# Kernel optimization log

Measured on AMD Instinct MI355X. Metric: run time of the kernel, lower is better.

Reference implementation:

```python
import jax, jax.numpy as jnp
import numpy as np

B = 2
SP = (480, 360, 32)   # spatial_shape (z, y, x)
GS = (8, 8, 8)        # query_gs_ratio
EP = (40, 15, 16)     # embed_params (pool compress ratio)
H = 8
N = 120000
D = 256
OUT = 20


def _dims(rat):
    return tuple((s + r - 1) // r for s, r in zip(SP, rat))


def sine_pe(coords, d_pos):
    # coords: [M,3] float voxel coords in original grid units; normalized sine PE
    nf = d_pos // 6
    sp = jnp.asarray(SP, jnp.float32)
    cn = coords / sp * (2.0 * jnp.pi)                      # normalize=True
    t = 10000.0 ** (jnp.arange(nf, dtype=jnp.float32) / nf)
    ang = cn[:, :, None] / t                               # [M,3,nf]
    pe = jnp.concatenate([jnp.sin(ang), jnp.cos(ang)], -1).reshape(coords.shape[0], -1)
    return jnp.pad(pe, ((0, 0), (0, d_pos - 6 * nf)))


def setup_inputs() -> dict:
    key = jax.random.key(0)
    ks = jax.random.split(key, 24)
    idx_b = jax.random.randint(ks[0], (N, 1), 0, B)
    idx_z = jax.random.randint(ks[1], (N, 1), 0, SP[0])
    idx_y = jax.random.randint(ks[2], (N, 1), 0, SP[1])
    idx_x = jax.random.randint(ks[3], (N, 1), 0, SP[2])
    indices = jnp.concatenate([idx_b, idx_z, idx_y, idx_x], axis=1).astype(jnp.int32)
    s = D ** -0.5
    p = lambda k, sh: jax.random.normal(k, sh, jnp.float32) * s
    return {
        'features': jax.random.normal(ks[4], (N, D), jnp.float32),
        'W_pool': p(ks[5], (D, D)), 'b_pool': jnp.zeros((D,), jnp.float32),
        'W_emb': p(ks[6], (D, D)), 'b_emb': jnp.zeros((D,), jnp.float32),
        'Wq': p(ks[7], (D, D)), 'bq': jnp.zeros((D,), jnp.float32),
        'Wk': p(ks[8], (D, D)), 'bk': jnp.zeros((D,), jnp.float32),
        'Wv': p(ks[9], (D, D)), 'bv': jnp.zeros((D,), jnp.float32),
        'Wo': p(ks[10], (D, D)), 'bo': jnp.zeros((D,), jnp.float32),
        'ln_g': jnp.ones((D,), jnp.float32), 'ln_b': jnp.zeros((D,), jnp.float32),
        'W_seg': p(ks[11], (D, OUT)), 'b_seg': jnp.zeros((OUT,), jnp.float32),
        'indices': indices,
        'batch_size': B,
    }


def reference(features, W_pool, b_pool, W_emb, b_emb, Wq, bq, Wk, bk, Wv, bv,
              Wo, bo, ln_g, ln_b, W_seg, b_seg, indices, batch_size):
    Zd, Yd, Xd = _dims(GS)
    Gq = Zd * Yd * Xd
    Sq = batch_size * Gq
    Ze, Ye, Xe = _dims(EP)
    Gk = Ze * Ye * Xe
    Sk = batch_size * Gk
    n = features.shape[0]

    # --- query pool branch: linear -> voxel-grid scatter_max ---
    pf = features @ W_pool + b_pool                                    # [N,D]
    dq = indices[:, 1:] // jnp.asarray(GS, jnp.int32)
    seg_q = ((indices[:, 0] * Zd + dq[:, 0]) * Yd + dq[:, 1]) * Xd + dq[:, 2]
    pool_max = jax.ops.segment_max(pf, seg_q, num_segments=Sq)
    cnt_q = jax.ops.segment_sum(jnp.ones((n,), jnp.float32), seg_q, num_segments=Sq)
    mq = cnt_q > 0
    pool_max = jnp.where(mq[:, None], pool_max, 0.0)
    cell = jnp.arange(Sq)
    rem = cell % Gq
    pool_c = jnp.stack([(rem // (Yd * Xd)) * GS[0],
                        ((rem // Xd) % Yd) * GS[1],
                        (rem % Xd) * GS[2]], -1).astype(jnp.float32)   # [Sq,3]

    # --- embedding branch ('pool'): linear -> coarse scatter_max + per-channel argmax coords ---
    ef = features @ W_emb + b_emb                                      # [N,D]
    de = indices[:, 1:] // jnp.asarray(EP, jnp.int32)
    seg_k = ((indices[:, 0] * Ze + de[:, 0]) * Ye + de[:, 1]) * Xe + de[:, 2]
    emb_max = jax.ops.segment_max(ef, seg_k, num_segments=Sk)
    cnt_k = jax.ops.segment_sum(jnp.ones((n,), jnp.float32), seg_k, num_segments=Sk)
    mk = cnt_k > 0
    emb_max = jnp.where(mk[:, None], emb_max, 0.0)
    winner = ef == jnp.where(mk[:, None], emb_max, -jnp.inf)[seg_k]
    idx = jax.ops.segment_max(jnp.where(winner, jnp.arange(n)[:, None], -1), seg_k, num_segments=Sk)
    idx_c = jnp.clip(idx, 0, n - 1)                                    # [Sk,D]
    ec = de.astype(jnp.float32)                                        # [N,3] downsampled coords
    emb_c = ec[idx_c].mean(axis=1) * jnp.asarray(EP, jnp.float32)      # [Sk,3]

    # --- position encoding (pointwise sine PE; per-batch loop in torch is pointwise-equivalent) ---
    pool_max = pool_max + sine_pe(pool_c, D)
    emb_max = emb_max + sine_pe(emb_c, D)

    # --- multi-head cross-attention (Q=pool, K/V=embedding), per-batch via dense grid reshape ---
    q_in = pool_max.reshape(batch_size, Gq, D)
    kv_in = emb_max.reshape(batch_size, Gk, D)
    dh = D // H
    q = (q_in @ Wq + bq).reshape(batch_size, Gq, H, dh)
    k = (kv_in @ Wk + bk).reshape(batch_size, Gk, H, dh)
    v = (kv_in @ Wv + bv).reshape(batch_size, Gk, H, dh)
    scores = jnp.einsum('bqhd,bkhd->bhqk', q, k) / jnp.float32(dh) ** 0.5
    kmask = mk.reshape(batch_size, Gk)
    scores = jnp.where(kmask[:, None, None, :], scores, -1e9)
    attn = jax.nn.softmax(scores, axis=-1)
    o = jnp.einsum('bhqk,bkhd->bqhd', attn, v).reshape(batch_size, Gq, D) @ Wo + bo
    h = q_in + o                                                       # residual + LayerNorm sublayer
    mu = h.mean(-1, keepdims=True)
    var = h.var(-1, keepdims=True)
    h = (h - mu) * jax.lax.rsqrt(var + 1e-5) * ln_g + ln_b
    feats_mhca = h.reshape(Sq, D)

    # --- gather back to voxels via pool_inv, residual, seg head (center-tap of SubMConv3d) ---
    vox = features + feats_mhca[seg_q]
    logits = vox @ W_seg + b_seg
    return logits
```

## Files before the change

### kernel.cpp

```cpp
#include <hip/hip_runtime.h>
#include <math.h>

#define N_PTS 120000
#define D 256
#define BATCH 2
#define NH 8
#define DH 32
#define OUTC 20

#define Zd 60
#define Yd 45
#define Xd 4
#define Gq 10800
#define Sq 21600

#define Ze 12
#define Ye 24
#define Xe 2
#define Gk 576
#define Sk 1152

#define QK_SCALE (0.17677669529663688f * 1.4426950408889634f)

typedef __bf16 bf16_t;
typedef __attribute__((ext_vector_type(8))) __bf16 bf16x8;
typedef __attribute__((ext_vector_type(4))) __bf16 bf16x4;
typedef __attribute__((ext_vector_type(4))) float f32x4;

__device__ __forceinline__ void glds16(const void* g, void* l) {
    __builtin_amdgcn_global_load_lds(
        (const __attribute__((address_space(1))) unsigned int*)g,
        (__attribute__((address_space(3))) unsigned int*)l,
        16, 0, 0);
}

__global__ __launch_bounds__(256) void k_prep(
    const float* __restrict__ Wp, const float* __restrict__ We,
    const float* __restrict__ Wq, const float* __restrict__ Wk,
    const float* __restrict__ Wv, const float* __restrict__ Wo,
    const float* __restrict__ bp, const float* __restrict__ be,
    const float* __restrict__ bq, const float* __restrict__ bk,
    const float* __restrict__ bv,
    const float* __restrict__ Wseg, const float* __restrict__ bseg,
    bf16_t* __restrict__ Wpe, bf16_t* __restrict__ Wqt,
    bf16_t* __restrict__ Wkv, bf16_t* __restrict__ Wot,
    bf16_t* __restrict__ Wsegt,
    float* __restrict__ bpe, float* __restrict__ bkv,
    float* __restrict__ bsegp, float* __restrict__ bqs)
{
    int n = blockIdx.x, k = threadIdx.x;
    if (n < 512) {
        const float* S = (n < 256) ? Wp : We;
        int nn = n & 255;
        Wpe[n * 256 + k] = (bf16_t)S[k * 256 + nn];
    } else if (n < 768) {
        int nn = n - 512;
        Wqt[nn * 256 + k] = (bf16_t)(Wq[k * 256 + nn] * QK_SCALE);
    } else if (n < 1280) {
        int m2 = n - 768;
        const float* S = (m2 < 256) ? Wk : Wv;
        int nn = m2 & 255;
        Wkv[m2 * 256 + k] = (bf16_t)S[k * 256 + nn];
    } else if (n < 1536) {
        int nn = n - 1280;
        Wot[nn * 256 + k] = (bf16_t)Wo[k * 256 + nn];
    } else if (n == 1536) {
        bpe[k] = bp[k]; bpe[256 + k] = be[k];
        bkv[k] = bk[k]; bkv[256 + k] = bv[k];
        bqs[k] = bq[k] * QK_SCALE;
        if (k < 32) bsegp[k] = (k < OUTC) ? bseg[k] : 0.f;
    } else {
        int n2 = n - 1537;
        Wsegt[n2 * 256 + k] = (n2 < OUTC) ? (bf16_t)Wseg[k * OUTC + n2] : (bf16_t)0.f;
    }
}

__global__ __launch_bounds__(256) void k_cast(
    const float* __restrict__ in, bf16_t* __restrict__ out)
{
    const size_t total = (size_t)N_PTS * 32;
    const size_t stride = (size_t)gridDim.x * 256;
    for (size_t i = (size_t)blockIdx.x * 256 + threadIdx.x; i < total; i += stride) {
        float4 a = *(const float4*)(in + i * 8);
        float4 b = *(const float4*)(in + i * 8 + 4);
        bf16x8 o;
        o[0] = (bf16_t)a.x; o[1] = (bf16_t)a.y; o[2] = (bf16_t)a.z; o[3] = (bf16_t)a.w;
        o[4] = (bf16_t)b.x; o[5] = (bf16_t)b.y; o[6] = (bf16_t)b.z; o[7] = (bf16_t)b.w;
        *(bf16x8*)(out + i * 8) = o;
    }
}

__global__ __launch_bounds__(256) void k_count(
    const int* __restrict__ indices, int* __restrict__ cnt_q, int* __restrict__ cnt_k,
    int* __restrict__ segq, int* __restrict__ segk)
{
    int i = blockIdx.x * 256 + threadIdx.x;
    if (i >= N_PTS) return;
    const int* id = indices + (size_t)i * 4;
    int b = id[0], z = id[1], y = id[2], x = id[3];
    int sq = ((b * Zd + (z >> 3)) * Yd + (y >> 3)) * Xd + (x >> 3);
    int sk = ((b * Ze + (z / 40)) * Ye + (y / 15)) * Xe + (x >> 4);
    segq[i] = sq; segk[i] = sk;
    atomicAdd(&cnt_q[sq], 1);
    atomicAdd(&cnt_k[sk], 1);
}

__global__ __launch_bounds__(1024) void k_scan(
    const int* __restrict__ cnt, int n, int* __restrict__ offs, int* __restrict__ cursor)
{
    __shared__ int wbase[17];
    __shared__ int carry_s;
    const int t = threadIdx.x, lane = t & 63, w = t >> 6;
    if (t == 0) carry_s = 0;
    __syncthreads();
    for (int base = 0; base < n; base += 1024) {
        int v = (base + t < n) ? cnt[base + t] : 0;
        int incl = v;
        #pragma unroll
        for (int off = 1; off < 64; off <<= 1) {
            int u = __shfl_up(incl, off);
            if (lane >= off) incl += u;
        }
        if (lane == 63) wbase[w + 1] = incl;
        __syncthreads();
        if (t == 0) {
            int s = 0;
            wbase[0] = 0;
            #pragma unroll
            for (int i = 1; i <= 16; ++i) { s += wbase[i]; wbase[i] = s; }
        }
        __syncthreads();
        int excl = incl - v + wbase[w] + carry_s;
        if (base + t < n) { offs[base + t] = excl; cursor[base + t] = excl; }
        __syncthreads();
        if (t == 0) carry_s += wbase[16];
        __syncthreads();
    }
}

__global__ __launch_bounds__(256) void k_place(
    const int* __restrict__ segq, const int* __restrict__ segk,
    int* __restrict__ cur_q, int* __restrict__ cur_k,
    int* __restrict__ ids_q, int* __restrict__ ids_k)
{
    int i = blockIdx.x * 256 + threadIdx.x;
    if (i >= N_PTS) return;
    ids_q[atomicAdd(&cur_q[segq[i]], 1)] = i;
    ids_k[atomicAdd(&cur_k[segk[i]], 1)] = i;
}

__global__ __launch_bounds__(256, 4) void k_gemm_bf(
    const bf16_t* __restrict__ A, int M,
    const bf16_t* __restrict__ Wt, const float* __restrict__ bias,
    bf16_t* __restrict__ outb, int ldo)
{
    __shared__ __align__(16) bf16_t Abuf[128 * 64];
    __shared__ __align__(16) bf16_t Bbuf[128 * 64];

    const int t = threadIdx.x;
    const int wave = t >> 6, lane = t & 63;
    const int wr = wave >> 1, wc = wave & 1;
    const int lrow = lane & 15, quad = lane >> 4;
    const int lr8 = lane >> 3, lc8 = lane & 7;
    const int row0 = blockIdx.y * 128;
    const int ntile = blockIdx.x;

    f32x4 acc[4][4];
    #pragma unroll
    for (int mi = 0; mi < 4; ++mi)
        #pragma unroll
        for (int ni = 0; ni < 4; ++ni)
            acc[mi][ni] = (f32x4){0.f, 0.f, 0.f, 0.f};

    for (int k0 = 0; k0 < 256; k0 += 64) {
        #pragma unroll
        for (int i = 0; i < 4; ++i) {
            int chunk = wave * 4 + i;
            int rowA = row0 + chunk * 8 + lr8;
            if (rowA > M - 1) rowA = M - 1;
            glds16(A + (size_t)rowA * 256 + k0 + lc8 * 8, &Abuf[chunk * 512]);
        }
        #pragma unroll
        for (int i = 0; i < 4; ++i) {
            int chunk = wave * 4 + i;
            glds16(Wt + (size_t)(ntile * 128 + chunk * 8 + lr8) * 256 + k0 + lc8 * 8,
                   &Bbuf[chunk * 512]);
        }
        asm volatile("s_waitcnt vmcnt(0)" ::: "memory");
        __builtin_amdgcn_sched_barrier(0);
        __syncthreads();

        #pragma unroll
        for (int kk = 0; kk < 64; kk += 32) {
            bf16x8 Af[4], Bf[4];
            #pragma unroll
            for (int mi = 0; mi < 4; ++mi)
                Af[mi] = *(const bf16x8*)&Abuf[(wr * 64 + mi * 16 + lrow) * 64 + kk + quad * 8];
            #pragma unroll
            for (int ni = 0; ni < 4; ++ni)
                Bf[ni] = *(const bf16x8*)&Bbuf[(wc * 64 + ni * 16 + lrow) * 64 + kk + quad * 8];
            #pragma unroll
            for (int mi = 0; mi < 4; ++mi)
                #pragma unroll
                for (int ni = 0; ni < 4; ++ni)
                    acc[mi][ni] = __builtin_amdgcn_mfma_f32_16x16x32_bf16(
                        Af[mi], Bf[ni], acc[mi][ni], 0, 0, 0);
        }
        __syncthreads();
    }

    const int colb = ntile * 128 + wc * 64;
    float biasv[4];
    #pragma unroll
    for (int ni = 0; ni < 4; ++ni) biasv[ni] = bias[colb + ni * 16 + lrow];

    #pragma unroll
    for (int mi = 0; mi < 4; ++mi) {
        int lr = wr * 64 + mi * 16 + quad * 4;
        #pragma unroll
        for (int reg = 0; reg < 4; ++reg) {
            int grow = row0 + lr + reg;
            if (grow >= M) continue;
            #pragma unroll
            for (int ni = 0; ni < 4; ++ni) {
                int col = colb + ni * 16 + lrow;
                outb[(size_t)grow * ldo + col] = (bf16_t)(acc[mi][ni][reg] + biasv[ni]);
            }
        }
    }
}

__global__ __launch_bounds__(512, 2) void k_gemm(
    const float* __restrict__ A, int M,
    const bf16_t* __restrict__ Wt, const float* __restrict__ bias,
    int mode, float* __restrict__ outp, int ldo)
{
    __shared__ __align__(16) bf16_t Abuf[128][72];
    __shared__ __align__(16) bf16_t Bbuf[256][72];

    const int t = threadIdx.x;
    const int wave = t >> 6, lane = t & 63;
    const int wr = wave >> 2, wc = wave & 3;
    const int lrow = lane & 15, quad = lane >> 4;
    const int row0 = blockIdx.y * 128;
    const int ntile = blockIdx.x;

    f32x4 acc[4][4];
    #pragma unroll
    for (int mi = 0; mi < 4; ++mi)
        #pragma unroll
        for (int ni = 0; ni < 4; ++ni)
            acc[mi][ni] = (f32x4){0.f, 0.f, 0.f, 0.f};

    for (int k0 = 0; k0 < 256; k0 += 64) {
        #pragma unroll
        for (int i = 0; i < 4; ++i) {
            int c = i * 512 + t;
            int r = c >> 4, c4 = c & 15;
            float4 v = make_float4(0.f, 0.f, 0.f, 0.f);
            if (row0 + r < M)
                v = *(const float4*)(A + (size_t)(row0 + r) * 256 + k0 + c4 * 4);
            bf16x4 bv4;
            bv4[0] = (bf16_t)v.x; bv4[1] = (bf16_t)v.y;
            bv4[2] = (bf16_t)v.z; bv4[3] = (bf16_t)v.w;
            *(bf16x4*)&Abuf[r][c4 * 4] = bv4;
        }
        #pragma unroll
        for (int i = 0; i < 4; ++i) {
            int c = i * 512 + t;
            int r = c >> 3, c8 = c & 7;
            uint4 w = *(const uint4*)(Wt + ((size_t)(ntile * 256 + r)) * 256 + k0 + c8 * 8);
            *(uint4*)&Bbuf[r][c8 * 8] = w;
        }
        __syncthreads();

        #pragma unroll
        for (int kk = 0; kk < 64; kk += 32) {
            bf16x8 Af[4], Bf[4];
            #pragma unroll
            for (int mi = 0; mi < 4; ++mi)
                Af[mi] = *(const bf16x8*)&Abuf[wr * 64 + mi * 16 + lrow][kk + quad * 8];
            #pragma unroll
            for (int ni = 0; ni < 4; ++ni)
                Bf[ni] = *(const bf16x8*)&Bbuf[wc * 64 + ni * 16 + lrow][kk + quad * 8];
            #pragma unroll
            for (int mi = 0; mi < 4; ++mi)
                #pragma unroll
                for (int ni = 0; ni < 4; ++ni)
                    acc[mi][ni] = __builtin_amdgcn_mfma_f32_16x16x32_bf16(
                        Af[mi], Bf[ni], acc[mi][ni], 0, 0, 0);
        }
        __syncthreads();
    }

    const int colb = ntile * 256 + wc * 64;
    float biasv[4];
    #pragma unroll
    for (int ni = 0; ni < 4; ++ni) biasv[ni] = bias[colb + ni * 16 + lrow];

    if (mode == 0) {
        #pragma unroll
        for (int mi = 0; mi < 4; ++mi) {
            int lr = wr * 64 + mi * 16 + quad * 4;
            #pragma unroll
            for (int reg = 0; reg < 4; ++reg) {
                int grow = row0 + lr + reg;
                if (grow >= M) continue;
                #pragma unroll
                for (int ni = 0; ni < 4; ++ni) {
                    int col = colb + ni * 16 + lrow;
                    outp[(size_t)grow * ldo + col] = acc[mi][ni][reg] + biasv[ni];
                }
            }
        }
    } else {
        bf16_t* outb = (bf16_t*)outp;
        #pragma unroll
        for (int mi = 0; mi < 4; ++mi) {
            int lr = wr * 64 + mi * 16 + quad * 4;
            #pragma unroll
            for (int reg = 0; reg < 4; ++reg) {
                int grow = row0 + lr + reg;
                if (grow >= M) continue;
                #pragma unroll
                for (int ni = 0; ni < 4; ++ni) {
                    int col = colb + ni * 16 + lrow;
                    outb[(size_t)grow * ldo + col] = (bf16_t)(acc[mi][ni][reg] + biasv[ni]);
                }
            }
        }
    }
}

__device__ inline float pe_val(int j, float cz, float cy, float cx) {
    if (j >= 252) return 0.f;
    int dim = j / 84;
    int f = j % 84;
    int fi = (f >= 42) ? (f - 42) : f;
    float c  = (dim == 0) ? cz : ((dim == 1) ? cy : cx);
    float sp = (dim == 0) ? 480.f : ((dim == 1) ? 360.f : 32.f);
    float cn = c / sp * 6.28318530717958647692f;
    float tt = expf((float)fi * (9.210340371976184f / 42.f));
    float ang = cn / tt;
    return (f >= 42) ? cosf(ang) : sinf(ang);
}

__global__ __launch_bounds__(256) void k_pool_q(
    const bf16_t* __restrict__ pfb, const int* __restrict__ ids,
    const int* __restrict__ offs, const int* __restrict__ cnt,
    float* __restrict__ out)
{
    const int t = threadIdx.x, lane = t & 63, w = t >> 6;
    const int s = blockIdx.x * 4 + w;
    if (s >= Sq) return;
    const int count = cnt[s], start = offs[s];
    float mx[4] = {-3.0e38f, -3.0e38f, -3.0e38f, -3.0e38f};
    for (int r = 0; r < count; ++r) {
        int i = ids[start + r];
        bf16x4 v = *(const bf16x4*)(pfb + (size_t)i * 256 + lane * 4);
        #pragma unroll
        for (int j = 0; j < 4; ++j) mx[j] = fmaxf(mx[j], (float)v[j]);
    }
    int rem = s % Gq;
    float cz = (float)((rem / (Yd * Xd)) * 8);
    float cy = (float)(((rem / Xd) % Yd) * 8);
    float cx = (float)((rem % Xd) * 8);
    #pragma unroll
    for (int j = 0; j < 4; ++j) {
        float v = (count > 0) ? mx[j] : 0.f;
        out[(size_t)s * 256 + lane * 4 + j] = v + pe_val(lane * 4 + j, cz, cy, cx);
    }
}

__global__ __launch_bounds__(512) void k_pool_k(
    const bf16_t* __restrict__ efb, const int* __restrict__ ids,
    const int* __restrict__ offs, const int* __restrict__ cnt,
    float* __restrict__ out, int* __restrict__ kmask)
{
    __shared__ float red[8][256];
    const int t = threadIdx.x, lane = t & 63, w = t >> 6;
    const int s = blockIdx.x;
    const int count = cnt[s], start = offs[s];
    float mx[4] = {-3.0e38f, -3.0e38f, -3.0e38f, -3.0e38f};
    for (int r = w; r < count; r += 8) {
        int i = ids[start + r];
        bf16x4 v = *(const bf16x4*)(efb + (size_t)i * 256 + lane * 4);
        #pragma unroll
        for (int j = 0; j < 4; ++j) mx[j] = fmaxf(mx[j], (float)v[j]);
    }
    #pragma unroll
    for (int j = 0; j < 4; ++j) red[w][lane * 4 + j] = mx[j];
    __syncthreads();
    if (t < 256) {
        float m = red[0][t];
        #pragma unroll
        for (int i = 1; i < 8; ++i) m = fmaxf(m, red[i][t]);
        if (count == 0) m = 0.f;
        int rem = s % Gk;
        float cz = (float)((rem / (Ye * Xe)) * 40);
        float cy = (float)(((rem / Xe) % Ye) * 15);
        float cx = (float)((rem % Xe) * 16);
        out[(size_t)s * 256 + t] = m + pe_val(t, cz, cy, cx);
        if (t == 0) kmask[s] = (count > 0) ? 1 : 0;
    }
}

__global__ __launch_bounds__(256) void k_vt(
    const bf16_t* __restrict__ KVb, bf16_t* __restrict__ VT)
{
    int idx = blockIdx.x * 256 + threadIdx.x;
    if (idx >= 16 * 32 * 576) return;
    int g = idx % 576;
    int d = (idx / 576) & 31;
    int bh = idx / (576 * 32);
    int b = bh >> 3, h = bh & 7;
    VT[idx] = KVb[((size_t)(b * Gk + g)) * 512 + 256 + h * 32 + d];
}

__global__ __launch_bounds__(768, 6) void k_attn5(
    const bf16_t* __restrict__ Q, const bf16_t* __restrict__ KV,
    const bf16_t* __restrict__ VT, const int* __restrict__ kmask,
    float* __restrict__ O)
{
    __shared__ __align__(16) bf16_t Vts[32][584];
    __shared__ __align__(16) bf16_t Ps[12][16][104];
    __shared__ float mskf[576];

    const int bh = blockIdx.y;
    const int b = bh >> 3, h = bh & 7;
    const int t = threadIdx.x, wave = t >> 6, lane = t & 63;
    const int lrow = lane & 15, quad = lane >> 4;
    const int q0 = blockIdx.x * 192;

    #pragma unroll
    for (int i = 0; i < 3; ++i) {
        int id = i * 768 + t;
        int d = id / 72, c8 = id % 72;
        uint4 v = *(const uint4*)(VT + (size_t)(bh * 32 + d) * 576 + c8 * 8);
        *(uint4*)&Vts[d][c8 * 8] = v;
    }
    if (t < 576)
        mskf[t] = kmask[b * Gk + t] ? 0.f : -1.0e9f;
    __syncthreads();

    int qa = q0 + wave * 16 + lrow;
    if (qa > Gq - 1) qa = Gq - 1;
    const bf16x8 Aq = *(const bf16x8*)(Q + ((size_t)(b * Gq + qa)) * 256 + h * 32 + quad * 8);

    const bf16_t* Kbase = KV + ((size_t)b * Gk) * 512 + h * 32;

    f32x4 oacc[2];
    oacc[0] = (f32x4){0.f, 0.f, 0.f, 0.f};
    oacc[1] = (f32x4){0.f, 0.f, 0.f, 0.f};
    float l[4] = {0.f, 0.f, 0.f, 0.f};

    for (int c0 = 0; c0 < Gk; c0 += 96) {
        #pragma unroll
        for (int nt = 0; nt < 6; ++nt) {
            bf16x8 Bk = *(const bf16x8*)(Kbase + (size_t)(c0 + nt * 16 + lrow) * 512 + quad * 8);
            f32x4 sacc = __builtin_amdgcn_mfma_f32_16x16x32_bf16(
                Aq, Bk, (f32x4){0.f, 0.f, 0.f, 0.f}, 0, 0, 0);
            float pen = mskf[c0 + nt * 16 + lrow];
            #pragma unroll
            for (int r = 0; r < 4; ++r) {
                float p = exp2f(sacc[r] + pen);
                l[r] += p;
                Ps[wave][quad * 4 + r][nt * 16 + lrow] = (bf16_t)p;
            }
        }
        #pragma unroll
        for (int ks = 0; ks < 3; ++ks) {
            bf16x8 Ap = *(const bf16x8*)&Ps[wave][lrow][ks * 32 + quad * 8];
            #pragma unroll
            for (int n2 = 0; n2 < 2; ++n2) {
                bf16x8 Bv = *(const bf16x8*)&Vts[n2 * 16 + lrow][c0 + ks * 32 + quad * 8];
                oacc[n2] = __builtin_amdgcn_mfma_f32_16x16x32_bf16(
                    Ap, Bv, oacc[n2], 0, 0, 0);
            }
        }
    }

    #pragma unroll
    for (int r = 0; r < 4; ++r)
        #pragma unroll
        for (int off = 1; off < 16; off <<= 1)
            l[r] += __shfl_xor(l[r], off);

    #pragma unroll
    for (int r = 0; r < 4; ++r) {
        int qi = q0 + wave * 16 + quad * 4 + r;
        if (qi >= Gq) continue;
        float inv = (l[r] > 0.f) ? (1.f / l[r]) : 0.f;
        #pragma unroll
        for (int n2 = 0; n2 < 2; ++n2)
            O[((size_t)(b * Gq + qi)) * 256 + h * 32 + n2 * 16 + lrow] = oacc[n2][r] * inv;
    }
}

__global__ __launch_bounds__(256) void k_ln(
    const float* __restrict__ oproj, const float* __restrict__ resid,
    const float* __restrict__ g, const float* __restrict__ bta,
    float* __restrict__ out)
{
    const int s = blockIdx.x, t = threadIdx.x;
    float h = resid[(size_t)s * D + t] + oproj[(size_t)s * D + t];

    float s1 = h, s2 = h * h;
    for (int o = 32; o > 0; o >>= 1) {
        s1 += __shfl_down(s1, o);
        s2 += __shfl_down(s2, o);
    }
    __shared__ float r1[4], r2[4];
    __shared__ float mu_s, rstd_s;
    int w = t >> 6;
    if ((t & 63) == 0) { r1[w] = s1; r2[w] = s2; }
    __syncthreads();
    if (t == 0) {
        float a = r1[0] + r1[1] + r1[2] + r1[3];
        float bsum = r2[0] + r2[1] + r2[2] + r2[3];
        float mu = a * (1.f / 256.f);
        float var = bsum * (1.f / 256.f) - mu * mu;
        mu_s = mu;
        rstd_s = rsqrtf(var + 1e-5f);
    }
    __syncthreads();
    out[(size_t)s * D + t] = (h - mu_s) * rstd_s * g[t] + bta[t];
}

__global__ __launch_bounds__(512, 2) void k_logits_mfma(
    const float* __restrict__ feat, const bf16_t* __restrict__ featb,
    const float* __restrict__ mhca,
    const int* __restrict__ indices, const bf16_t* __restrict__ Wsegt,
    const float* __restrict__ bsegp, float* __restrict__ out)
{
    __shared__ __align__(16) bf16_t Abuf[128][72];
    __shared__ __align__(16) bf16_t Bbuf[32][72];
    __shared__ int sq_s[128];

    const int t = threadIdx.x;
    const int wave = t >> 6, lane = t & 63;
    const int lrow = lane & 15, quad = lane >> 4;
    const int row0 = blockIdx.x * 128;

    if (t < 128) {
        int row = row0 + t;
        if (row < N_PTS) {
            const int* id = indices + (size_t)row * 4;
            sq_s[t] = ((id[0] * Zd + (id[1] >> 3)) * Yd + (id[2] >> 3)) * Xd + (id[3] >> 3);
        } else sq_s[t] = 0;
    }
    __syncthreads();

    f32x4 acc[2];
    acc[0] = (f32x4){0.f, 0.f, 0.f, 0.f};
    acc[1] = (f32x4){0.f, 0.f, 0.f, 0.f};

    for (int k0 = 0; k0 < 256; k0 += 64) {
        #pragma unroll
        for (int i = 0; i < 4; ++i) {
            int c = i * 512 + t;
            int r = c >> 4, c4 = c & 15;
            float4 v = make_float4(0.f, 0.f, 0.f, 0.f);
            int grow = row0 + r;
            if (grow < N_PTS) {
                float4 mm = *(const float4*)(mhca + (size_t)sq_s[r] * 256 + k0 + c4 * 4);
                if (featb) {
                    bf16x4 fv = *(const bf16x4*)(featb + (size_t)grow * 256 + k0 + c4 * 4);
                    v.x = (float)fv[0] + mm.x; v.y = (float)fv[1] + mm.y;
                    v.z = (float)fv[2] + mm.z; v.w = (float)fv[3] + mm.w;
                } else {
                    v = *(const float4*)(feat + (size_t)grow * 256 + k0 + c4 * 4);
                    v.x += mm.x; v.y += mm.y; v.z += mm.z; v.w += mm.w;
                }
            }
            bf16x4 bv4;
            bv4[0] = (bf16_t)v.x; bv4[1] = (bf16_t)v.y;
            bv4[2] = (bf16_t)v.z; bv4[3] = (bf16_t)v.w;
            *(bf16x4*)&Abuf[r][c4 * 4] = bv4;
        }
        if (t < 256) {
            int r = t >> 3, c8 = t & 7;
            uint4 w = *(const uint4*)(Wsegt + (size_t)r * 256 + k0 + c8 * 8);
            *(uint4*)&Bbuf[r][c8 * 8] = w;
        }
        __syncthreads();

        #pragma unroll
        for (int kk = 0; kk < 64; kk += 32) {
            bf16x8 Af = *(const bf16x8*)&Abuf[wave * 16 + lrow][kk + quad * 8];
            #pragma unroll
            for (int ni = 0; ni < 2; ++ni) {
                bf16x8 Bf = *(const bf16x8*)&Bbuf[ni * 16 + lrow][kk + quad * 8];
                acc[ni] = __builtin_amdgcn_mfma_f32_16x16x32_bf16(
                    Af, Bf, acc[ni], 0, 0, 0);
            }
        }
        __syncthreads();
    }

    #pragma unroll
    for (int ni = 0; ni < 2; ++ni) {
        int col = ni * 16 + lrow;
        if (col >= OUTC) continue;
        float bias = bsegp[col];
        #pragma unroll
        for (int reg = 0; reg < 4; ++reg) {
            int grow = row0 + wave * 16 + quad * 4 + reg;
            if (grow >= N_PTS) continue;
            out[(size_t)grow * OUTC + col] = acc[ni][reg] + bias;
        }
    }
}

extern "C" void kernel_launch(void* const* d_in, const int* in_sizes, int n_in,
                              void* d_out, int out_size, void* d_ws, size_t ws_size,
                              hipStream_t stream) {
    const float* features = (const float*)d_in[0];
    const float* W_pool = (const float*)d_in[1];
    const float* b_pool = (const float*)d_in[2];
    const float* W_emb  = (const float*)d_in[3];
    const float* b_emb  = (const float*)d_in[4];
    const float* Wq = (const float*)d_in[5];
    const float* bq = (const float*)d_in[6];
    const float* Wk = (const float*)d_in[7];
    const float* bk = (const float*)d_in[8];
    const float* Wv = (const float*)d_in[9];
    const float* bv = (const float*)d_in[10];
    const float* Wo = (const float*)d_in[11];
    const float* bo = (const float*)d_in[12];
    const float* ln_g = (const float*)d_in[13];
    const float* ln_b = (const float*)d_in[14];
    const float* W_seg = (const float*)d_in[15];
    const float* b_seg = (const float*)d_in[16];
    const int* indices = (const int*)d_in[17];
    float* out = (float*)d_out;

    float* ws = (float*)d_ws;
    const size_t SQD = (size_t)Sq * D;
    const size_t SKD = (size_t)Sk * D;
    const size_t PFB_FL = (size_t)N_PTS * D / 2;

    size_t oP   = 0;
    size_t oPF  = oP + PFB_FL;
    size_t oEF  = oPF + SQD;
    size_t oWpe = oEF + SKD;
    size_t oWqt = oWpe + 65536;
    size_t oWkv = oWqt + 32768;
    size_t oWot = oWkv + 65536;
    size_t obpe = oWot + 32768;
    size_t obkv = obpe + 512;
    size_t oCnt = obkv + 512;
    size_t oOffq = oCnt + 21600 + 1152;
    size_t oCurq = oOffq + 21600;
    size_t oOffk = oCurq + 21600;
    size_t oCurk = oOffk + 1152;
    size_t oSegq = oCurk + 1152;
    size_t oSegk = oSegq + N_PTS;
    size_t oIdsq = oSegk + N_PTS;
    size_t oIdsk = oIdsq + N_PTS;
    size_t oKm   = oIdsk + N_PTS;
    size_t oWst  = oKm + 1152;
    size_t obsg  = oWst + 4096;
    size_t obqs  = obsg + 32;
    size_t oFB   = obqs + 256;

    bf16_t* pfb = (bf16_t*)(ws + oP);
    float* pool_feat = ws + oPF;
    float* emb_feat  = ws + oEF;
    bf16_t* Wpe = (bf16_t*)(ws + oWpe);
    bf16_t* Wqt = (bf16_t*)(ws + oWqt);
    bf16_t* Wkv = (bf16_t*)(ws + oWkv);
    bf16_t* Wot = (bf16_t*)(ws + oWot);
    float* bpe = ws + obpe;
    float* bkv = ws + obkv;
    int* cnt_q = (int*)(ws + oCnt);
    int* cnt_k = cnt_q + 21600;
    int* offs_q = (int*)(ws + oOffq);
    int* cur_q  = (int*)(ws + oCurq);
    int* offs_k = (int*)(ws + oOffk);
    int* cur_k  = (int*)(ws + oCurk);
    int* segq = (int*)(ws + oSegq);
    int* segk = (int*)(ws + oSegk);
    int* ids_q = (int*)(ws + oIdsq);
    int* ids_k = (int*)(ws + oIdsk);
    int* kmask = (int*)(ws + oKm);
    bf16_t* Wsegt = (bf16_t*)(ws + oWst);
    float* bsegp = ws + obsg;
    float* bqs = ws + obqs;
    bf16_t* fb16 = (bf16_t*)(ws + oFB);

    bf16_t* Qb  = (bf16_t*)(ws + oP);
    bf16_t* KVb = (bf16_t*)(ws + oP + 2764800);
    float* attnO = ws + oP + 3059712;
    float* oproj = ws + oP + 8589312;
    float* mhca  = ws + oP + 3059712;
    bf16_t* VT = (bf16_t*)(ws + oEF);

    const bool fast = ws_size >= (oFB + PFB_FL) * sizeof(float);

    hipMemsetAsync(cnt_q, 0, (21600 + 1152) * sizeof(int), stream);

    k_prep<<<1569, 256, 0, stream>>>(W_pool, W_emb, Wq, Wk, Wv, Wo,
                                     b_pool, b_emb, bq, bk, bv, W_seg, b_seg,
                                     Wpe, Wqt, Wkv, Wot, Wsegt, bpe, bkv, bsegp, bqs);

    if (fast)
        k_cast<<<2048, 256, 0, stream>>>(features, fb16);

    k_count<<<(N_PTS + 255) / 256, 256, 0, stream>>>(indices, cnt_q, cnt_k, segq, segk);
    k_scan<<<1, 1024, 0, stream>>>(cnt_q, 21600, offs_q, cur_q);
    k_scan<<<1, 1024, 0, stream>>>(cnt_k, 1152, offs_k, cur_k);
    k_place<<<(N_PTS + 255) / 256, 256, 0, stream>>>(segq, segk, cur_q, cur_k, ids_q, ids_k);

    if (fast) {
        dim3 g(2, (N_PTS + 127) / 128);
        k_gemm_bf<<<g, 256, 0, stream>>>(fb16, N_PTS, Wpe + 256 * 256, bpe + 256,
                                         pfb, 256);
    } else {
        dim3 g(1, (N_PTS + 127) / 128);
        k_gemm<<<g, 512, 0, stream>>>(features, N_PTS, Wpe + 256 * 256, bpe + 256, 2,
                                      (float*)pfb, 256);
    }
    k_pool_k<<<Sk, 512, 0, stream>>>(pfb, ids_k, offs_k, cnt_k, emb_feat, kmask);

    if (fast) {
        dim3 g(2, (N_PTS + 127) / 128);
        k_gemm_bf<<<g, 256, 0, stream>>>(fb16, N_PTS, Wpe, bpe, pfb, 256);
    } else {
        dim3 g(1, (N_PTS + 127) / 128);
        k_gemm<<<g, 512, 0, stream>>>(features, N_PTS, Wpe, bpe, 2,
                                      (float*)pfb, 256);
    }
    k_pool_q<<<(Sq + 3) / 4, 256, 0, stream>>>(pfb, ids_q, offs_q, cnt_q, pool_feat);

    {
        dim3 g(1, (Sq + 127) / 128);
        k_gemm<<<g, 512, 0, stream>>>(pool_feat, Sq, Wqt, bqs, 2, (float*)Qb, 256);
    }
    {
        dim3 g(2, (Sk + 127) / 128);
        k_gemm<<<g, 512, 0, stream>>>(emb_feat, Sk, Wkv, bkv, 2, (float*)KVb, 512);
    }

    k_vt<<<(16 * 32 * 576 + 255) / 256, 256, 0, stream>>>(KVb, VT);

    {
        dim3 ag((Gq + 191) / 192, BATCH * NH);
        k_attn5<<<ag, 768, 0, stream>>>(Qb, KVb, VT, kmask, attnO);
    }

    {
        dim3 g(1, (Sq + 127) / 128);
        k_gemm<<<g, 512, 0, stream>>>(attnO, Sq, Wot, bo, 0, oproj, 256);
    }

    k_ln<<<Sq, 256, 0, stream>>>(oproj, pool_feat, ln_g, ln_b, mhca);

    k_logits_mfma<<<(N_PTS + 127) / 128, 512, 0, stream>>>(
        features, fast ? fb16 : (const bf16_t*)nullptr, mhca, indices, Wsegt, bsegp, out);
}
```

Measured before the change: 575.0 us.

## Carry bf16 intermediates through attention path and use glds GEMMs for Q, O-proj, logits

The pooled query features, attention output and LayerNorm output are now written as bf16 instead of fp32. The Q projection and output projection move onto the bf16 direct-to-LDS GEMM kernel, which gains an fp32-output option. A new logits kernel loads bf16 features and gathered mhca rows straight into LDS and accumulates both through MFMA, so it no longer converts fp32 inputs in registers. This cuts memory traffic and conversion work, at the cost of extra rounding of intermediates to bf16.

```diff
diff --git a/kernel.cpp b/kernel.cpp
--- a/kernel.cpp
+++ b/kernel.cpp
@@ -152,7 +152,7 @@
 __global__ __launch_bounds__(256, 4) void k_gemm_bf(
     const bf16_t* __restrict__ A, int M,
     const bf16_t* __restrict__ Wt, const float* __restrict__ bias,
-    bf16_t* __restrict__ outb, int ldo)
+    void* __restrict__ outp, int ldo, int fp32out)
 {
     __shared__ __align__(16) bf16_t Abuf[128 * 64];
     __shared__ __align__(16) bf16_t Bbuf[128 * 64];
@@ -224,7 +224,11 @@
             #pragma unroll
             for (int ni = 0; ni < 4; ++ni) {
                 int col = colb + ni * 16 + lrow;
-                outb[(size_t)grow * ldo + col] = (bf16_t)(acc[mi][ni][reg] + biasv[ni]);
+                float val = acc[mi][ni][reg] + biasv[ni];
+                if (fp32out)
+                    ((float*)outp)[(size_t)grow * ldo + col] = val;
+                else
+                    ((bf16_t*)outp)[(size_t)grow * ldo + col] = (bf16_t)val;
             }
         }
     }
@@ -348,7 +352,7 @@
 __global__ __launch_bounds__(256) void k_pool_q(
     const bf16_t* __restrict__ pfb, const int* __restrict__ ids,
     const int* __restrict__ offs, const int* __restrict__ cnt,
-    float* __restrict__ out)
+    float* __restrict__ out, bf16_t* __restrict__ outb)
 {
     const int t = threadIdx.x, lane = t & 63, w = t >> 6;
     const int s = blockIdx.x * 4 + w;
@@ -365,11 +369,15 @@
     float cz = (float)((rem / (Yd * Xd)) * 8);
     float cy = (float)(((rem / Xd) % Yd) * 8);
     float cx = (float)((rem % Xd) * 8);
+    bf16x4 ob;
     #pragma unroll
     for (int j = 0; j < 4; ++j) {
         float v = (count > 0) ? mx[j] : 0.f;
-        out[(size_t)s * 256 + lane * 4 + j] = v + pe_val(lane * 4 + j, cz, cy, cx);
-    }
+        float o = v + pe_val(lane * 4 + j, cz, cy, cx);
+        out[(size_t)s * 256 + lane * 4 + j] = o;
+        ob[j] = (bf16_t)o;
+    }
+    *(bf16x4*)(outb + (size_t)s * 256 + lane * 4) = ob;
 }
 
 __global__ __launch_bounds__(512) void k_pool_k(
@@ -420,7 +428,7 @@
 __global__ __launch_bounds__(768, 6) void k_attn5(
     const bf16_t* __restrict__ Q, const bf16_t* __restrict__ KV,
     const bf16_t* __restrict__ VT, const int* __restrict__ kmask,
-    float* __restrict__ O)
+    bf16_t* __restrict__ O)
 {
     __shared__ __align__(16) bf16_t Vts[32][584];
     __shared__ __align__(16) bf16_t Ps[12][16][104];
@@ -493,14 +501,15 @@
         float inv = (l[r] > 0.f) ? (1.f / l[r]) : 0.f;
         #pragma unroll
         for (int n2 = 0; n2 < 2; ++n2)
-            O[((size_t)(b * Gq + qi)) * 256 + h * 32 + n2 * 16 + lrow] = oacc[n2][r] * inv;
+            O[((size_t)(b * Gq + qi)) * 256 + h * 32 + n2 * 16 + lrow] =
+                (bf16_t)(oacc[n2][r] * inv);
     }
 }
 
 __global__ __launch_bounds__(256) void k_ln(
     const float* __restrict__ oproj, const float* __restrict__ resid,
     const float* __restrict__ g, const float* __restrict__ bta,
-    float* __restrict__ out)
+    bf16_t* __restrict__ out)
 {
     const int s = blockIdx.x, t = threadIdx.x;
     float h = resid[(size_t)s * D + t] + oproj[(size_t)s * D + t];
@@ -524,12 +533,102 @@
         rstd_s = rsqrtf(var + 1e-5f);
     }
     __syncthreads();
-    out[(size_t)s * D + t] = (h - mu_s) * rstd_s * g[t] + bta[t];
+    out[(size_t)s * D + t] = (bf16_t)((h - mu_s) * rstd_s * g[t] + bta[t]);
+}
+
+__global__ __launch_bounds__(256, 4) void k_logits_glds(
+    const bf16_t* __restrict__ featb, const bf16_t* __restrict__ mhcab,
+    const int* __restrict__ indices, const bf16_t* __restrict__ Wsegt,
+    const float* __restrict__ bsegp, float* __restrict__ out)
+{
+    __shared__ __align__(16) bf16_t Fbuf[128 * 64];
+    __shared__ __align__(16) bf16_t Mbuf[128 * 64];
+    __shared__ __align__(16) bf16_t Bbuf[32 * 64];
+    __shared__ int sq_s[128];
+
+    const int t = threadIdx.x;
+    const int wave = t >> 6, lane = t & 63;
+    const int lrow = lane & 15, quad = lane >> 4;
+    const int lr8 = lane >> 3, lc8 = lane & 7;
+    const int row0 = blockIdx.x * 128;
+
+    if (t < 128) {
+        int row = row0 + t;
+        if (row >= N_PTS) row = N_PTS - 1;
+        const int* id = indices + (size_t)row * 4;
+        sq_s[t] = ((id[0] * Zd + (id[1] >> 3)) * Yd + (id[2] >> 3)) * Xd + (id[3] >> 3);
+    }
+    __syncthreads();
+
+    f32x4 acc[2][2];
+    #pragma unroll
+    for (int mi = 0; mi < 2; ++mi)
+        #pragma unroll
+        for (int ni = 0; ni < 2; ++ni)
+            acc[mi][ni] = (f32x4){0.f, 0.f, 0.f, 0.f};
+
+    for (int k0 = 0; k0 < 256; k0 += 64) {
+        #pragma unroll
+        for (int i = 0; i < 4; ++i) {
+            int chunk = wave * 4 + i;
+            int rowA = row0 + chunk * 8 + lr8;
+            if (rowA > N_PTS - 1) rowA = N_PTS - 1;
+            glds16(featb + (size_t)rowA * 256 + k0 + lc8 * 8, &Fbuf[chunk * 512]);
+        }
+        #pragma unroll
+        for (int i = 0; i < 4; ++i) {
+            int chunk = wave * 4 + i;
+            int mrow = sq_s[chunk * 8 + lr8];
+            glds16(mhcab + (size_t)mrow * 256 + k0 + lc8 * 8, &Mbuf[chunk * 512]);
+        }
+        glds16(Wsegt + (size_t)(wave * 8 + lr8) * 256 + k0 + lc8 * 8, &Bbuf[wave * 512]);
+
+        asm volatile("s_waitcnt vmcnt(0)" ::: "memory");
+        __builtin_amdgcn_sched_barrier(0);
+        __syncthreads();
+
+        #pragma unroll
+        for (int kk = 0; kk < 64; kk += 32) {
+            bf16x8 Bf[2];
+            #pragma unroll
+            for (int ni = 0; ni < 2; ++ni)
+                Bf[ni] = *(const bf16x8*)&Bbuf[(ni * 16 + lrow) * 64 + kk + quad * 8];
+            #pragma unroll
+            for (int mi = 0; mi < 2; ++mi) {
+                int arow = wave * 32 + mi * 16 + lrow;
+                bf16x8 Ff = *(const bf16x8*)&Fbuf[arow * 64 + kk + quad * 8];
+                bf16x8 Mf = *(const bf16x8*)&Mbuf[arow * 64 + kk + quad * 8];
+                #pragma unroll
+                for (int ni = 0; ni < 2; ++ni) {
+                    acc[mi][ni] = __builtin_amdgcn_mfma_f32_16x16x32_bf16(
+                        Ff, Bf[ni], acc[mi][ni], 0, 0, 0);
+                    acc[mi][ni] = __builtin_amdgcn_mfma_f32_16x16x32_bf16(
+                        Mf, Bf[ni], acc[mi][ni], 0, 0, 0);
+                }
+            }
+        }
+        __syncthreads();
+    }
+
+    #pragma unroll
+    for (int ni = 0; ni < 2; ++ni) {
+        int col = ni * 16 + lrow;
+        if (col >= OUTC) continue;
+        float bias = bsegp[col];
+        #pragma unroll
+        for (int mi = 0; mi < 2; ++mi) {
+            #pragma unroll
+            for (int reg = 0; reg < 4; ++reg) {
+                int grow = row0 + wave * 32 + mi * 16 + quad * 4 + reg;
+                if (grow >= N_PTS) continue;
+                out[(size_t)grow * OUTC + col] = acc[mi][ni][reg] + bias;
+            }
+        }
+    }
 }
 
 __global__ __launch_bounds__(512, 2) void k_logits_mfma(
-    const float* __restrict__ feat, const bf16_t* __restrict__ featb,
-    const float* __restrict__ mhca,
+    const float* __restrict__ feat, const bf16_t* __restrict__ mhcab,
     const int* __restrict__ indices, const bf16_t* __restrict__ Wsegt,
     const float* __restrict__ bsegp, float* __restrict__ out)
 {
@@ -563,15 +662,10 @@
             float4 v = make_float4(0.f, 0.f, 0.f, 0.f);
             int grow = row0 + r;
             if (grow < N_PTS) {
-                float4 mm = *(const float4*)(mhca + (size_t)sq_s[r] * 256 + k0 + c4 * 4);
-                if (featb) {
-                    bf16x4 fv = *(const bf16x4*)(featb + (size_t)grow * 256 + k0 + c4 * 4);
-                    v.x = (float)fv[0] + mm.x; v.y = (float)fv[1] + mm.y;
-                    v.z = (float)fv[2] + mm.z; v.w = (float)fv[3] + mm.w;
-                } else {
-                    v = *(const float4*)(feat + (size_t)grow * 256 + k0 + c4 * 4);
-                    v.x += mm.x; v.y += mm.y; v.z += mm.z; v.w += mm.w;
-                }
+                v = *(const float4*)(feat + (size_t)grow * 256 + k0 + c4 * 4);
+                bf16x4 mv = *(const bf16x4*)(mhcab + (size_t)sq_s[r] * 256 + k0 + c4 * 4);
+                v.x += (float)mv[0]; v.y += (float)mv[1];
+                v.z += (float)mv[2]; v.w += (float)mv[3];
             }
             bf16x4 bv4;
             bv4[0] = (bf16_t)v.x; bv4[1] = (bf16_t)v.y;
@@ -639,6 +733,7 @@
     const size_t SQD = (size_t)Sq * D;
     const size_t SKD = (size_t)Sk * D;
     const size_t PFB_FL = (size_t)N_PTS * D / 2;
+    const size_t SQB_FL = (size_t)Sq * D / 2;
 
     size_t oP   = 0;
     size_t oPF  = oP + PFB_FL;
@@ -662,7 +757,8 @@
     size_t oWst  = oKm + 1152;
     size_t obsg  = oWst + 4096;
     size_t obqs  = obsg + 32;
-    size_t oFB   = obqs + 256;
+    size_t oPFB  = obqs + 256;
+    size_t oFB   = oPFB + SQB_FL;
 
     bf16_t* pfb = (bf16_t*)(ws + oP);
     float* pool_feat = ws + oPF;
@@ -687,13 +783,14 @@
     bf16_t* Wsegt = (bf16_t*)(ws + oWst);
     float* bsegp = ws + obsg;
     float* bqs = ws + obqs;
+    bf16_t* pool_featb = (bf16_t*)(ws + oPFB);
     bf16_t* fb16 = (bf16_t*)(ws + oFB);
 
     bf16_t* Qb  = (bf16_t*)(ws + oP);
     bf16_t* KVb = (bf16_t*)(ws + oP + 2764800);
-    float* attnO = ws + oP + 3059712;
+    bf16_t* Ob  = (bf16_t*)(ws + oP + 3059712);
     float* oproj = ws + oP + 8589312;
-    float* mhca  = ws + oP + 3059712;
+    bf16_t* mhcab = (bf16_t*)(ws + oP + 3059712);
     bf16_t* VT = (bf16_t*)(ws + oEF);
 
     const bool fast = ws_size >= (oFB + PFB_FL) * sizeof(float);
@@ -715,7 +812,7 @@
     if (fast) {
         dim3 g(2, (N_PTS + 127) / 128);
         k_gemm_bf<<<g, 256, 0, stream>>>(fb16, N_PTS, Wpe + 256 * 256, bpe + 256,
-                                         pfb, 256);
+                                         pfb, 256, 0);
     } else {
         dim3 g(1, (N_PTS + 127) / 128);
         k_gemm<<<g, 512, 0, stream>>>(features, N_PTS, Wpe + 256 * 256, bpe + 256, 2,
@@ -725,17 +822,18 @@
 
     if (fast) {
         dim3 g(2, (N_PTS + 127) / 128);
-        k_gemm_bf<<<g, 256, 0, stream>>>(fb16, N_PTS, Wpe, bpe, pfb, 256);
+        k_gemm_bf<<<g, 256, 0, stream>>>(fb16, N_PTS, Wpe, bpe, pfb, 256, 0);
     } else {
         dim3 g(1, (N_PTS + 127) / 128);
         k_gemm<<<g, 512, 0, stream>>>(features, N_PTS, Wpe, bpe, 2,
                                       (float*)pfb, 256);
     }
-    k_pool_q<<<(Sq + 3) / 4, 256, 0, stream>>>(pfb, ids_q, offs_q, cnt_q, pool_feat);
+    k_pool_q<<<(Sq + 3) / 4, 256, 0, stream>>>(pfb, ids_q, offs_q, cnt_q,
+                                               pool_feat, pool_featb);
 
     {
-        dim3 g(1, (Sq + 127) / 128);
-        k_gemm<<<g, 512, 0, stream>>>(pool_feat, Sq, Wqt, bqs, 2, (float*)Qb, 256);
+        dim3 g(2, (Sq + 127) / 128);
+        k_gemm_bf<<<g, 256, 0, stream>>>(pool_featb, Sq, Wqt, bqs, Qb, 256, 0);
     }
     {
         dim3 g(2, (Sk + 127) / 128);
@@ -746,16 +844,20 @@
 
     {
         dim3 ag((Gq + 191) / 192, BATCH * NH);
-        k_attn5<<<ag, 768, 0, stream>>>(Qb, KVb, VT, kmask, attnO);
+        k_attn5<<<ag, 768, 0, stream>>>(Qb, KVb, VT, kmask, Ob);
     }
 
     {
-        dim3 g(1, (Sq + 127) / 128);
-        k_gemm<<<g, 512, 0, stream>>>(attnO, Sq, Wot, bo, 0, oproj, 256);
-    }
-
-    k_ln<<<Sq, 256, 0, stream>>>(oproj, pool_feat, ln_g, ln_b, mhca);
-
-    k_logits_mfma<<<(N_PTS + 127) / 128, 512, 0, stream>>>(
-        features, fast ? fb16 : (const bf16_t*)nullptr, mhca, indices, Wsegt, bsegp, out);
-}
+        dim3 g(2, (Sq + 127) / 128);
+        k_gemm_bf<<<g, 256, 0, stream>>>(Ob, Sq, Wot, bo, oproj, 256, 1);
+    }
+
+    k_ln<<<Sq, 256, 0, stream>>>(oproj, pool_feat, ln_g, ln_b, mhcab);
+
+    if (fast)
+        k_logits_glds<<<(N_PTS + 127) / 128, 256, 0, stream>>>(
+            fb16, mhcab, indices, Wsegt, bsegp, out);
+    else
+        k_logits_mfma<<<(N_PTS + 127) / 128, 512, 0, stream>>>(
+            features, mhcab, indices, Wsegt, bsegp, out);
+}
```

Measured after the change: 588.4 us. 2.3% more time.

## Carry bf16 intermediates through Q-proj, attention output, O-proj and LayerNorm

Applied to the files above, without the earlier changes.

Pooled query features, the attention output and the LayerNorm output are now also stored in bf16. The Q and O projections switch from the fp32-input GEMM to the bf16-input GEMM, which gains an fp32-output option. This is meant to cut memory traffic and the in-kernel fp32-to-bf16 conversion in those GEMMs, and to halve the gather bandwidth in the logits kernel. It costs an extra bf16 write in k_pool_q and extra rounding of intermediates.

```diff
diff --git a/kernel.cpp b/kernel.cpp
--- a/kernel.cpp
+++ b/kernel.cpp
@@ -152,7 +152,7 @@
 __global__ __launch_bounds__(256, 4) void k_gemm_bf(
     const bf16_t* __restrict__ A, int M,
     const bf16_t* __restrict__ Wt, const float* __restrict__ bias,
-    bf16_t* __restrict__ outb, int ldo)
+    void* __restrict__ outp, int ldo, int fp32out)
 {
     __shared__ __align__(16) bf16_t Abuf[128 * 64];
     __shared__ __align__(16) bf16_t Bbuf[128 * 64];
@@ -224,7 +224,11 @@
             #pragma unroll
             for (int ni = 0; ni < 4; ++ni) {
                 int col = colb + ni * 16 + lrow;
-                outb[(size_t)grow * ldo + col] = (bf16_t)(acc[mi][ni][reg] + biasv[ni]);
+                float val = acc[mi][ni][reg] + biasv[ni];
+                if (fp32out)
+                    ((float*)outp)[(size_t)grow * ldo + col] = val;
+                else
+                    ((bf16_t*)outp)[(size_t)grow * ldo + col] = (bf16_t)val;
             }
         }
     }
@@ -348,7 +352,7 @@
 __global__ __launch_bounds__(256) void k_pool_q(
     const bf16_t* __restrict__ pfb, const int* __restrict__ ids,
     const int* __restrict__ offs, const int* __restrict__ cnt,
-    float* __restrict__ out)
+    float* __restrict__ out, bf16_t* __restrict__ outb)
 {
     const int t = threadIdx.x, lane = t & 63, w = t >> 6;
     const int s = blockIdx.x * 4 + w;
@@ -365,11 +369,15 @@
     float cz = (float)((rem / (Yd * Xd)) * 8);
     float cy = (float)(((rem / Xd) % Yd) * 8);
     float cx = (float)((rem % Xd) * 8);
+    bf16x4 ob;
     #pragma unroll
     for (int j = 0; j < 4; ++j) {
         float v = (count > 0) ? mx[j] : 0.f;
-        out[(size_t)s * 256 + lane * 4 + j] = v + pe_val(lane * 4 + j, cz, cy, cx);
-    }
+        float o = v + pe_val(lane * 4 + j, cz, cy, cx);
+        out[(size_t)s * 256 + lane * 4 + j] = o;
+        ob[j] = (bf16_t)o;
+    }
+    *(bf16x4*)(outb + (size_t)s * 256 + lane * 4) = ob;
 }
 
 __global__ __launch_bounds__(512) void k_pool_k(
@@ -420,7 +428,7 @@
 __global__ __launch_bounds__(768, 6) void k_attn5(
     const bf16_t* __restrict__ Q, const bf16_t* __restrict__ KV,
     const bf16_t* __restrict__ VT, const int* __restrict__ kmask,
-    float* __restrict__ O)
+    bf16_t* __restrict__ O)
 {
     __shared__ __align__(16) bf16_t Vts[32][584];
     __shared__ __align__(16) bf16_t Ps[12][16][104];
@@ -493,14 +501,15 @@
         float inv = (l[r] > 0.f) ? (1.f / l[r]) : 0.f;
         #pragma unroll
         for (int n2 = 0; n2 < 2; ++n2)
-            O[((size_t)(b * Gq + qi)) * 256 + h * 32 + n2 * 16 + lrow] = oacc[n2][r] * inv;
+            O[((size_t)(b * Gq + qi)) * 256 + h * 32 + n2 * 16 + lrow] =
+                (bf16_t)(oacc[n2][r] * inv);
     }
 }
 
 __global__ __launch_bounds__(256) void k_ln(
     const float* __restrict__ oproj, const float* __restrict__ resid,
     const float* __restrict__ g, const float* __restrict__ bta,
-    float* __restrict__ out)
+    bf16_t* __restrict__ out)
 {
     const int s = blockIdx.x, t = threadIdx.x;
     float h = resid[(size_t)s * D + t] + oproj[(size_t)s * D + t];
@@ -524,12 +533,12 @@
         rstd_s = rsqrtf(var + 1e-5f);
     }
     __syncthreads();
-    out[(size_t)s * D + t] = (h - mu_s) * rstd_s * g[t] + bta[t];
+    out[(size_t)s * D + t] = (bf16_t)((h - mu_s) * rstd_s * g[t] + bta[t]);
 }
 
 __global__ __launch_bounds__(512, 2) void k_logits_mfma(
     const float* __restrict__ feat, const bf16_t* __restrict__ featb,
-    const float* __restrict__ mhca,
+    const bf16_t* __restrict__ mhcab,
     const int* __restrict__ indices, const bf16_t* __restrict__ Wsegt,
     const float* __restrict__ bsegp, float* __restrict__ out)
 {
@@ -563,14 +572,15 @@
             float4 v = make_float4(0.f, 0.f, 0.f, 0.f);
             int grow = row0 + r;
             if (grow < N_PTS) {
-                float4 mm = *(const float4*)(mhca + (size_t)sq_s[r] * 256 + k0 + c4 * 4);
+                bf16x4 mv = *(const bf16x4*)(mhcab + (size_t)sq_s[r] * 256 + k0 + c4 * 4);
                 if (featb) {
                     bf16x4 fv = *(const bf16x4*)(featb + (size_t)grow * 256 + k0 + c4 * 4);
-                    v.x = (float)fv[0] + mm.x; v.y = (float)fv[1] + mm.y;
-                    v.z = (float)fv[2] + mm.z; v.w = (float)fv[3] + mm.w;
+                    v.x = (float)fv[0] + (float)mv[0]; v.y = (float)fv[1] + (float)mv[1];
+                    v.z = (float)fv[2] + (float)mv[2]; v.w = (float)fv[3] + (float)mv[3];
                 } else {
                     v = *(const float4*)(feat + (size_t)grow * 256 + k0 + c4 * 4);
-                    v.x += mm.x; v.y += mm.y; v.z += mm.z; v.w += mm.w;
+                    v.x += (float)mv[0]; v.y += (float)mv[1];
+                    v.z += (float)mv[2]; v.w += (float)mv[3];
                 }
             }
             bf16x4 bv4;
@@ -639,6 +649,7 @@
     const size_t SQD = (size_t)Sq * D;
     const size_t SKD = (size_t)Sk * D;
     const size_t PFB_FL = (size_t)N_PTS * D / 2;
+    const size_t SQB_FL = (size_t)Sq * D / 2;
 
     size_t oP   = 0;
     size_t oPF  = oP + PFB_FL;
@@ -662,7 +673,8 @@
     size_t oWst  = oKm + 1152;
     size_t obsg  = oWst + 4096;
     size_t obqs  = obsg + 32;
-    size_t oFB   = obqs + 256;
+    size_t oPFB  = obqs + 256;
+    size_t oFB   = oPFB + SQB_FL;
 
     bf16_t* pfb = (bf16_t*)(ws + oP);
     float* pool_feat = ws + oPF;
@@ -687,13 +699,14 @@
     bf16_t* Wsegt = (bf16_t*)(ws + oWst);
     float* bsegp = ws + obsg;
     float* bqs = ws + obqs;
+    bf16_t* pool_featb = (bf16_t*)(ws + oPFB);
     bf16_t* fb16 = (bf16_t*)(ws + oFB);
 
     bf16_t* Qb  = (bf16_t*)(ws + oP);
     bf16_t* KVb = (bf16_t*)(ws + oP + 2764800);
-    float* attnO = ws + oP + 3059712;
+    bf16_t* Ob  = (bf16_t*)(ws + oP + 3059712);
     float* oproj = ws + oP + 8589312;
-    float* mhca  = ws + oP + 3059712;
+    bf16_t* mhcab = (bf16_t*)(ws + oP + 3059712);
     bf16_t* VT = (bf16_t*)(ws + oEF);
 
     const bool fast = ws_size >= (oFB + PFB_FL) * sizeof(float);
@@ -715,7 +728,7 @@
     if (fast) {
         dim3 g(2, (N_PTS + 127) / 128);
         k_gemm_bf<<<g, 256, 0, stream>>>(fb16, N_PTS, Wpe + 256 * 256, bpe + 256,
-                                         pfb, 256);
+                                         pfb, 256, 0);
     } else {
         dim3 g(1, (N_PTS + 127) / 128);
         k_gemm<<<g, 512, 0, stream>>>(features, N_PTS, Wpe + 256 * 256, bpe + 256, 2,
@@ -725,17 +738,18 @@
 
     if (fast) {
         dim3 g(2, (N_PTS + 127) / 128);
-        k_gemm_bf<<<g, 256, 0, stream>>>(fb16, N_PTS, Wpe, bpe, pfb, 256);
+        k_gemm_bf<<<g, 256, 0, stream>>>(fb16, N_PTS, Wpe, bpe, pfb, 256, 0);
     } else {
         dim3 g(1, (N_PTS + 127) / 128);
         k_gemm<<<g, 512, 0, stream>>>(features, N_PTS, Wpe, bpe, 2,
                                       (float*)pfb, 256);
     }
-    k_pool_q<<<(Sq + 3) / 4, 256, 0, stream>>>(pfb, ids_q, offs_q, cnt_q, pool_feat);
+    k_pool_q<<<(Sq + 3) / 4, 256, 0, stream>>>(pfb, ids_q, offs_q, cnt_q,
+                                               pool_feat, pool_featb);
 
     {
-        dim3 g(1, (Sq + 127) / 128);
-        k_gemm<<<g, 512, 0, stream>>>(pool_feat, Sq, Wqt, bqs, 2, (float*)Qb, 256);
+        dim3 g(2, (Sq + 127) / 128);
+        k_gemm_bf<<<g, 256, 0, stream>>>(pool_featb, Sq, Wqt, bqs, Qb, 256, 0);
     }
     {
         dim3 g(2, (Sk + 127) / 128);
@@ -746,16 +760,17 @@
 
     {
         dim3 ag((Gq + 191) / 192, BATCH * NH);
-        k_attn5<<<ag, 768, 0, stream>>>(Qb, KVb, VT, kmask, attnO);
+        k_attn5<<<ag, 768, 0, stream>>>(Qb, KVb, VT, kmask, Ob);
     }
 
     {
-        dim3 g(1, (Sq + 127) / 128);
-        k_gemm<<<g, 512, 0, stream>>>(attnO, Sq, Wot, bo, 0, oproj, 256);
-    }
-
-    k_ln<<<Sq, 256, 0, stream>>>(oproj, pool_feat, ln_g, ln_b, mhca);
+        dim3 g(2, (Sq + 127) / 128);
+        k_gemm_bf<<<g, 256, 0, stream>>>(Ob, Sq, Wot, bo, oproj, 256, 1);
+    }
+
+    k_ln<<<Sq, 256, 0, stream>>>(oproj, pool_feat, ln_g, ln_b, mhcab);
 
     k_logits_mfma<<<(N_PTS + 127) / 128, 512, 0, stream>>>(
-        features, fast ? fb16 : (const bf16_t*)nullptr, mhca, indices, Wsegt, bsegp, out);
-}
+        features, fast ? fb16 : (const bf16_t*)nullptr, mhcab,
+        indices, Wsegt, bsegp, out);
+}
```

Measured after the change: 588.9 us. 2.4% more time.
